# Kernel optimization log

Hardware: AMD Instinct MI355X
Metric: run time of the kernel (lower is better)

Reference implementation:

```python
import jax, jax.numpy as jnp
import numpy as np

HIDDEN = 1024
HEADS = 16
HEAD_DIM = HIDDEN // HEADS


def setup_inputs() -> dict:
    key = jax.random.key(0)
    kx, kw = jax.random.split(key)
    x = jax.random.normal(kx, (1, 4096, HIDDEN), dtype=jnp.float32)
    # torch Linear weight is [out, in]; we store as [in, out] for x @ W
    W_qkv = jax.random.normal(kw, (HIDDEN, 3 * HIDDEN), dtype=jnp.float32) * (HIDDEN ** -0.5)
    return {"x": x, "W_qkv": W_qkv}


def reference(x, W_qkv):
    B, T, _ = x.shape
    qkv = x @ W_qkv                                    # [B, T, 3*HIDDEN]
    qkv = qkv.reshape(B, T, 3, HEADS, HEAD_DIM)
    qkv = jnp.transpose(qkv, (2, 0, 3, 1, 4))          # [3, B, H, T, Dh]
    q, k, v = qkv[0], qkv[1], qkv[2]
    scale = HEAD_DIM ** -0.5
    attn = jnp.einsum("bhqd,bhkd->bhqk", q, k) * scale  # [B, H, T, T] materialized (naive)
    attn = jax.nn.softmax(attn, axis=-1)
    out = jnp.einsum("bhqk,bhkd->bhqd", attn, v)        # [B, H, T, Dh]
    out = jnp.transpose(out, (0, 2, 1, 3)).reshape(B, T, HIDDEN)
    return out
```

## Files before the change

kernel.cpp:

```cpp
#include <hip/hip_runtime.h>

#define SEQ 4096
#define HID 1024
#define NH  16
#define DH  64
#define N3  3072

typedef __attribute__((ext_vector_type(4))) float floatx4;
typedef __attribute__((ext_vector_type(8))) short shortx8;
typedef __attribute__((ext_vector_type(4))) short shortx4;

__device__ __forceinline__ short f2bf(float f) {
    return (short)((__builtin_bit_cast(unsigned, f) + 0x8000u) >> 16);
}
__device__ __forceinline__ unsigned pk2bf(float a, float b) {
    unsigned ua = __builtin_bit_cast(unsigned, a) + 0x8000u;
    unsigned ub = __builtin_bit_cast(unsigned, b) + 0x8000u;
    return (ua >> 16) | (ub & 0xFFFF0000u);
}
__device__ __forceinline__ shortx4 pk4bf(float a, float b, float c, float d) {
    union { unsigned u[2]; shortx4 s; } x;
    x.u[0] = pk2bf(a, b);
    x.u[1] = pk2bf(c, d);
    return x.s;
}

__device__ __forceinline__ unsigned cvtpk(float lo, float hi) {
    unsigned r;
    asm("v_cvt_pk_bf16_f32 %0, %1, %2" : "=v"(r) : "v"(lo), "v"(hi));
    return r;
}

#if __has_builtin(__builtin_amdgcn_exp2f)
#define fexp2 __builtin_amdgcn_exp2f
#else
#define fexp2 exp2f
#endif

#define mfma32 __builtin_amdgcn_mfma_f32_16x16x32_bf16

__device__ __forceinline__ void gll16(const short* g, short* l) {
    __builtin_amdgcn_global_load_lds(
        (const __attribute__((address_space(1))) unsigned*)g,
        (__attribute__((address_space(3))) unsigned*)l, 16, 0, 0);
}

__global__ __launch_bounds__(256) void convert_x(
    const float* __restrict__ x, short* __restrict__ Xb)
{
    size_t i = (size_t)blockIdx.x * 256 + threadIdx.x;
    float4 v = *(const float4*)&x[i * 4];
    shortx4 b = pk4bf(v.x, v.y, v.z, v.w);
    *(shortx4*)&Xb[i * 4] = b;
}

__global__ __launch_bounds__(256) void transpose_W(
    const float* __restrict__ W, short* __restrict__ Wt)
{
    __shared__ short Ws[128 * 40];
    const int t  = threadIdx.x;
    const int n0 = blockIdx.x * 128;
    const int k0 = blockIdx.y * 32;
    #pragma unroll
    for (int i = 0; i < 4; i++) {
        int idx = t + i * 256;
        int k = idx >> 5, c4 = idx & 31;
        float4 v = *(const float4*)&W[(size_t)(k0 + k) * N3 + n0 + c4 * 4];
        Ws[(c4 * 4 + 0) * 40 + k] = f2bf(v.x);
        Ws[(c4 * 4 + 1) * 40 + k] = f2bf(v.y);
        Ws[(c4 * 4 + 2) * 40 + k] = f2bf(v.z);
        Ws[(c4 * 4 + 3) * 40 + k] = f2bf(v.w);
    }
    __syncthreads();
    #pragma unroll
    for (int i = 0; i < 2; i++) {
        int idx = t + i * 256;
        int n = idx >> 2, seg = idx & 3;
        shortx8 g = *(const shortx8*)&Ws[n * 40 + seg * 8];
        *(shortx8*)&Wt[(size_t)(n0 + n) * HID + k0 + seg * 8] = g;
    }
}

#define LDC 136
__global__ __launch_bounds__(256) void qkv_gemm(
    const short* __restrict__ Xb, const short* __restrict__ Wt,
    short* __restrict__ Qb, short* __restrict__ Kb, short* __restrict__ Vb)
{
    __shared__ short SM[18432];
    short* As = SM;
    short* Bs = SM + 128 * 64;
    const int tid  = threadIdx.x;
    const int m0   = blockIdx.x * 128;
    const int n0   = blockIdx.y * 128;
    const int lane = tid & 63;
    const int wid  = tid >> 6;
    const int wm   = (wid >> 1) * 64;
    const int wn   = (wid & 1) * 64;
    const int l15  = lane & 15;
    const int quad = lane >> 4;

    floatx4 acc[4][4];
    #pragma unroll
    for (int i = 0; i < 4; i++)
        #pragma unroll
        for (int j = 0; j < 4; j++)
            acc[i][j] = (floatx4){0.f, 0.f, 0.f, 0.f};

    const int arow = tid >> 3, ac = tid & 7;
    const int swk  = (ac ^ (arow & 7)) << 3;
    const short* ag = Xb + (size_t)(m0 + arow) * HID + swk;
    const short* bg = Wt + (size_t)(n0 + arow) * HID + swk;
    short* al = As + (size_t)(tid & 192) * 8;
    short* bl = Bs + (size_t)(tid & 192) * 8;
    const int r7 = l15 & 7;

    for (int k0 = 0; k0 < HID; k0 += 64) {
        #pragma unroll
        for (int i = 0; i < 4; i++)
            gll16(ag + (size_t)i * 32 * HID + k0, al + i * 2048);
        #pragma unroll
        for (int i = 0; i < 4; i++)
            gll16(bg + (size_t)i * 32 * HID + k0, bl + i * 2048);
        __syncthreads();
        #pragma unroll
        for (int kh = 0; kh < 2; kh++) {
            shortx8 af[4], bf[4];
            #pragma unroll
            for (int t = 0; t < 4; t++) {
                int R = wm + t * 16 + l15;
                af[t] = *(const shortx8*)&As[(R << 6) + ((((kh << 2) + quad) ^ r7) << 3)];
                int Rb = wn + t * 16 + l15;
                bf[t] = *(const shortx8*)&Bs[(Rb << 6) + ((((kh << 2) + quad) ^ r7) << 3)];
            }
            #pragma unroll
            for (int tm = 0; tm < 4; tm++)
                #pragma unroll
                for (int tn = 0; tn < 4; tn++)
                    acc[tm][tn] = mfma32(af[tm], bf[tn], acc[tm][tn], 0, 0, 0);
        }
        __syncthreads();
    }

    short* Cs = SM;
    const float sc = (n0 < 1024) ? 0.18033688011112042f : 1.0f;
    #pragma unroll
    for (int tm = 0; tm < 4; tm++)
        #pragma unroll
        for (int tn = 0; tn < 4; tn++)
            #pragma unroll
            for (int r = 0; r < 4; r++)
                Cs[(wm + tm * 16 + quad * 4 + r) * LDC + wn + tn * 16 + l15] =
                    f2bf(acc[tm][tn][r] * sc);
    __syncthreads();
    short* base = (n0 < 1024) ? Qb : (n0 < 2048 ? Kb : Vb);
    const int h0 = (n0 & 1023) >> 6;
    #pragma unroll
    for (int j = 0; j < 8; j++) {
        int idx = tid + j * 256;
        int row = idx >> 4, col = (idx & 15) * 8;
        shortx8 v = *(const shortx8*)&Cs[row * LDC + col];
        *(shortx8*)&base[((size_t)(h0 + (col >> 6)) * SEQ + m0 + row) * DH + (col & 63)] = v;
    }
}

__global__ __launch_bounds__(256) void transpose_V(
    const short* __restrict__ Vb, short* __restrict__ Vt)
{
    __shared__ short Ts[64 * 72];
    const int t  = threadIdx.x;
    const int t0 = blockIdx.x * 64;
    const int h  = blockIdx.y;
    #pragma unroll
    for (int i = 0; i < 2; i++) {
        int idx = t + i * 256;
        int r = idx >> 3, seg = idx & 7;
        shortx8 g = *(const shortx8*)&Vb[((size_t)h * SEQ + t0 + r) * DH + seg * 8];
        *(shortx8*)&Ts[r * 72 + seg * 8] = g;
    }
    __syncthreads();
    #pragma unroll
    for (int i = 0; i < 2; i++) {
        int idx = t + i * 256;
        int d = idx >> 3, tseg = idx & 7;
        shortx8 g;
        #pragma unroll
        for (int j = 0; j < 8; j++) g[j] = Ts[(tseg * 8 + j) * 72 + d];
        *(shortx8*)&Vt[((size_t)h * DH + d) * SEQ + t0 + tseg * 8] = g;
    }
}

__global__ __launch_bounds__(256) void flash_attn(
    const short* __restrict__ Qb, const short* __restrict__ Kb,
    const short* __restrict__ Vt, float* __restrict__ out,
    float* __restrict__ Opart, float* __restrict__ Lpart,
    int kpc, int nit, int final)
{
    __shared__ short Ks[2][4096];
    __shared__ short Vs[2][4096];
    const int tid  = threadIdx.x;
    const int lane = tid & 63;
    const int l15  = lane & 15;
    const int quad = lane >> 4;

    const int nblk = (int)(gridDim.x * gridDim.y * gridDim.z);
    const int lin  = (int)blockIdx.x + ((int)blockIdx.y << 5) + ((int)blockIdx.z << 9);
    const int work = (lin & 7) * (nblk >> 3) + (lin >> 3);
    const int h    = (work >> 5) & 15;
    const int ch   = work >> 9;
    const int q0   = (work & 31) * 128 + (tid >> 6) * 32;
    const int tstart = ch * kpc;
    const shortx8 ones8 = {(short)0x3F80, (short)0x3F80, (short)0x3F80, (short)0x3F80,
                           (short)0x3F80, (short)0x3F80, (short)0x3F80, (short)0x3F80};

    const short* qp = Qb + ((size_t)h * SEQ + q0 + l15) * DH;
    shortx8 qf00 = *(const shortx8*)(qp + quad * 8);
    shortx8 qf01 = *(const shortx8*)(qp + 32 + quad * 8);
    shortx8 qf10 = *(const shortx8*)(qp + 16 * DH + quad * 8);
    shortx8 qf11 = *(const shortx8*)(qp + 16 * DH + 32 + quad * 8);

    floatx4 oacc[2][4];
    #pragma unroll
    for (int s = 0; s < 2; s++)
        #pragma unroll
        for (int dn = 0; dn < 4; dn++)
            oacc[s][dn] = (floatx4){0.f, 0.f, 0.f, 0.f};
    floatx4 lacc0 = {0.f, 0.f, 0.f, 0.f}, lacc1 = {0.f, 0.f, 0.f, 0.f};

    const int rK   = tid >> 3, sK = tid & 7;
    const int key0 = 8 * ((rK >> 2) & 3) + 4 * ((rK >> 4) & 1) + (rK & 3);
    const int swo  = (sK ^ (rK & 7)) << 3;
    const short* kg = Kb + ((size_t)h * SEQ + tstart + key0) * DH + swo;
    const short* vg = Vt + ((size_t)h * DH + rK) * SEQ + tstart + swo;
    const int wslot = (tid & 192) * 8;

    gll16(kg,            &Ks[0][wslot]);
    gll16(kg + 32 * DH,  &Ks[0][wslot + 2048]);
    gll16(vg,            &Vs[0][wslot]);
    gll16(vg + 32 * SEQ, &Vs[0][wslot + 2048]);
    kg += 64 * DH;  vg += 64;

    for (int it = 0; it < nit; it++) {
        __syncthreads();
        if (it + 1 < nit) {
            int b = (it + 1) & 1;
            gll16(kg,            &Ks[b][wslot]);
            gll16(kg + 32 * DH,  &Ks[b][wslot + 2048]);
            gll16(vg,            &Vs[b][wslot]);
            gll16(vg + 32 * SEQ, &Vs[b][wslot + 2048]);
            kg += 64 * DH;  vg += 64;
        }
        const short* ks = Ks[it & 1];
        const short* vs = Vs[it & 1];

        floatx4 st0[4], st1[4];
        __builtin_amdgcn_s_setprio(1);
        #pragma unroll
        for (int tn = 0; tn < 4; tn++) {
            int R = tn * 16 + l15;
            int off = (R << 6) + ((quad ^ (R & 7)) << 3);
            shortx8 kf0 = *(const shortx8*)&ks[off];
            shortx8 kf1 = *(const shortx8*)&ks[off ^ 32];
            floatx4 a0 = {0.f, 0.f, 0.f, 0.f};
            a0 = mfma32(kf0, qf00, a0, 0, 0, 0);
            a0 = mfma32(kf1, qf01, a0, 0, 0, 0);
            st0[tn] = a0;
            floatx4 a1 = {0.f, 0.f, 0.f, 0.f};
            a1 = mfma32(kf0, qf10, a1, 0, 0, 0);
            a1 = mfma32(kf1, qf11, a1, 0, 0, 0);
            st1[tn] = a1;
        }
        __builtin_amdgcn_s_setprio(0);

        union { unsigned u[4]; shortx8 s; } pa00, pa01, pa10, pa11;
        #pragma unroll
        for (int half = 0; half < 2; half++) {
            int ta = half * 2, tb = half * 2 + 1;
            unsigned* d0 = half ? pa01.u : pa00.u;
            unsigned* d1 = half ? pa11.u : pa10.u;
            d0[0] = cvtpk(fexp2(st0[ta][0]), fexp2(st0[ta][1]));
            d0[1] = cvtpk(fexp2(st0[ta][2]), fexp2(st0[ta][3]));
            d0[2] = cvtpk(fexp2(st0[tb][0]), fexp2(st0[tb][1]));
            d0[3] = cvtpk(fexp2(st0[tb][2]), fexp2(st0[tb][3]));
            d1[0] = cvtpk(fexp2(st1[ta][0]), fexp2(st1[ta][1]));
            d1[1] = cvtpk(fexp2(st1[ta][2]), fexp2(st1[ta][3]));
            d1[2] = cvtpk(fexp2(st1[tb][0]), fexp2(st1[tb][1]));
            d1[3] = cvtpk(fexp2(st1[tb][2]), fexp2(st1[tb][3]));
        }

        __builtin_amdgcn_s_setprio(1);
        lacc0 = mfma32(pa00.s, ones8, lacc0, 0, 0, 0);
        lacc0 = mfma32(pa01.s, ones8, lacc0, 0, 0, 0);
        lacc1 = mfma32(pa10.s, ones8, lacc1, 0, 0, 0);
        lacc1 = mfma32(pa11.s, ones8, lacc1, 0, 0, 0);

        #pragma unroll
        for (int dn = 0; dn < 4; dn++) {
            int row = dn * 16 + l15;
            int off = (row << 6) + ((quad ^ (row & 7)) << 3);
            shortx8 va = *(const shortx8*)&vs[off];
            shortx8 vb = *(const shortx8*)&vs[off ^ 32];
            oacc[0][dn] = mfma32(pa00.s, va, oacc[0][dn], 0, 0, 0);
            oacc[0][dn] = mfma32(pa01.s, vb, oacc[0][dn], 0, 0, 0);
            oacc[1][dn] = mfma32(pa10.s, va, oacc[1][dn], 0, 0, 0);
            oacc[1][dn] = mfma32(pa11.s, vb, oacc[1][dn], 0, 0, 0);
        }
        __builtin_amdgcn_s_setprio(0);
    }

    if (final) {
        #pragma unroll
        for (int r = 0; r < 4; r++) {
            float rl0 = 1.0f / lacc0[r], rl1 = 1.0f / lacc1[r];
            int query = q0 + quad * 4 + r;
            float* d0 = out + (size_t)query * HID + h * DH + l15;
            float* d1 = d0 + (size_t)16 * HID;
            #pragma unroll
            for (int dn = 0; dn < 4; dn++) {
                d0[dn * 16] = oacc[0][dn][r] * rl0;
                d1[dn * 16] = oacc[1][dn][r] * rl1;
            }
        }
    } else {
        #pragma unroll
        for (int r = 0; r < 4; r++) {
            int query = q0 + quad * 4 + r;
            float* d0 = Opart + ((size_t)ch * SEQ + query) * HID + h * DH + l15;
            float* d1 = d0 + (size_t)16 * HID;
            #pragma unroll
            for (int dn = 0; dn < 4; dn++) {
                d0[dn * 16] = oacc[0][dn][r];
                d1[dn * 16] = oacc[1][dn][r];
            }
        }
        if (l15 == 0) {
            float* lp = Lpart + ((size_t)ch * NH + h) * SEQ + q0;
            #pragma unroll
            for (int r = 0; r < 4; r++) {
                lp[quad * 4 + r]      = lacc0[r];
                lp[16 + quad * 4 + r] = lacc1[r];
            }
        }
    }
}

__global__ __launch_bounds__(256) void combine(
    const float* __restrict__ Opart, const float* __restrict__ Lpart,
    float* __restrict__ out, int chn)
{
    size_t i = ((size_t)blockIdx.x * 256 + threadIdx.x) * 4;
    int q = (int)(i >> 10);
    int h = ((int)i & 1023) >> 6;
    float4 o = {0.f, 0.f, 0.f, 0.f};
    float l = 0.f;
    for (int c = 0; c < chn; c++) {
        float4 p = *(const float4*)&Opart[(size_t)c * SEQ * HID + i];
        o.x += p.x; o.y += p.y; o.z += p.z; o.w += p.w;
        l += Lpart[((size_t)c * NH + h) * SEQ + q];
    }
    float rl = 1.0f / l;
    float4 r = {o.x * rl, o.y * rl, o.z * rl, o.w * rl};
    *(float4*)&out[i] = r;
}

extern "C" void kernel_launch(void* const* d_in, const int* in_sizes, int n_in,
                              void* d_out, int out_size, void* d_ws, size_t ws_size,
                              hipStream_t stream) {
    const float* x = (const float*)d_in[0];
    const float* W = (const float*)d_in[1];
    float* out = (float*)d_out;

    short* Xb = (short*)d_ws;
    short* Wt = Xb + (size_t)SEQ * HID;
    short* Qb = Wt + (size_t)N3 * HID;
    short* Kb = Qb + (size_t)NH * SEQ * DH;
    short* Vb = Kb + (size_t)NH * SEQ * DH;
    short* Vt = Xb;
    float* Opart = (float*)(Vb + (size_t)NH * SEQ * DH);

    const size_t need = 39845888ull
                      + 2ull * SEQ * HID * 4
                      + 2ull * NH * SEQ * 4;
    const int chn = (ws_size >= need) ? 2 : 1;
    float* Lpart = Opart + (size_t)chn * SEQ * HID;
    const int kpc = SEQ / chn, nit = kpc / 64;

    convert_x  <<<dim3(SEQ * HID / 1024), 256, 0, stream>>>(x, Xb);
    transpose_W<<<dim3(N3 / 128, HID / 32), 256, 0, stream>>>(W, Wt);
    qkv_gemm   <<<dim3(SEQ / 128, N3 / 128), 256, 0, stream>>>(Xb, Wt, Qb, Kb, Vb);
    transpose_V<<<dim3(SEQ / 64, NH), 256, 0, stream>>>(Vb, Vt);
    flash_attn <<<dim3(SEQ / 128, NH, chn), 256, 0, stream>>>(
        Qb, Kb, Vt, out, Opart, Lpart, kpc, nit, chn == 1);
    if (chn > 1)
        combine<<<dim3(SEQ * HID / 1024), 256, 0, stream>>>(Opart, Lpart, out, chn);
}
```

Baseline: 201.6 us.

## Use two waves of 64 queries per block to double K/V fragment reuse

The flash attention block drops from four waves of 32 queries to two waves of 64 queries each. Every K and V fragment read from shared memory now feeds twice as many MFMAs, which halves LDS read traffic per unit of compute. Each thread now issues eight global-to-LDS loads per stage instead of four. The cost is more accumulator and Q registers per wave and fewer waves per block, which can reduce occupancy and the ability to hide latency.

```diff
diff --git a/kernel.cpp b/kernel.cpp
--- a/kernel.cpp
+++ b/kernel.cpp
@@ -189,7 +189,7 @@
     }
 }
 
-__global__ __launch_bounds__(256) void flash_attn(
+__global__ __launch_bounds__(128, 2) void flash_attn(
     const short* __restrict__ Qb, const short* __restrict__ Kb,
     const short* __restrict__ Vt, float* __restrict__ out,
     float* __restrict__ Opart, float* __restrict__ Lpart,
@@ -198,6 +198,7 @@
     __shared__ short Ks[2][4096];
     __shared__ short Vs[2][4096];
     const int tid  = threadIdx.x;
+    const int wid  = tid >> 6;
     const int lane = tid & 63;
     const int l15  = lane & 15;
     const int quad = lane >> 4;
@@ -207,91 +208,97 @@
     const int work = (lin & 7) * (nblk >> 3) + (lin >> 3);
     const int h    = (work >> 5) & 15;
     const int ch   = work >> 9;
-    const int q0   = (work & 31) * 128 + (tid >> 6) * 32;
+    const int q0   = (work & 31) * 128 + wid * 64;
     const int tstart = ch * kpc;
     const shortx8 ones8 = {(short)0x3F80, (short)0x3F80, (short)0x3F80, (short)0x3F80,
                            (short)0x3F80, (short)0x3F80, (short)0x3F80, (short)0x3F80};
-
-    const short* qp = Qb + ((size_t)h * SEQ + q0 + l15) * DH;
-    shortx8 qf00 = *(const shortx8*)(qp + quad * 8);
-    shortx8 qf01 = *(const shortx8*)(qp + 32 + quad * 8);
-    shortx8 qf10 = *(const shortx8*)(qp + 16 * DH + quad * 8);
-    shortx8 qf11 = *(const shortx8*)(qp + 16 * DH + 32 + quad * 8);
-
-    floatx4 oacc[2][4];
-    #pragma unroll
-    for (int s = 0; s < 2; s++)
+    const floatx4 z4 = {0.f, 0.f, 0.f, 0.f};
+
+    shortx8 qf[4][2];
+    #pragma unroll
+    for (int s = 0; s < 4; s++) {
+        const short* qp = Qb + ((size_t)h * SEQ + q0 + s * 16 + l15) * DH;
+        qf[s][0] = *(const shortx8*)(qp + quad * 8);
+        qf[s][1] = *(const shortx8*)(qp + 32 + quad * 8);
+    }
+
+    floatx4 oacc[4][4];
+    #pragma unroll
+    for (int s = 0; s < 4; s++)
         #pragma unroll
         for (int dn = 0; dn < 4; dn++)
-            oacc[s][dn] = (floatx4){0.f, 0.f, 0.f, 0.f};
-    floatx4 lacc0 = {0.f, 0.f, 0.f, 0.f}, lacc1 = {0.f, 0.f, 0.f, 0.f};
+            oacc[s][dn] = z4;
+    floatx4 lacc[4] = {z4, z4, z4, z4};
 
     const int rK   = tid >> 3, sK = tid & 7;
-    const int key0 = 8 * ((rK >> 2) & 3) + 4 * ((rK >> 4) & 1) + (rK & 3);
+    const int key0 = 8 * ((rK >> 2) & 3) + (rK & 3);
     const int swo  = (sK ^ (rK & 7)) << 3;
     const short* kg = Kb + ((size_t)h * SEQ + tstart + key0) * DH + swo;
     const short* vg = Vt + ((size_t)h * DH + rK) * SEQ + tstart + swo;
-    const int wslot = (tid & 192) * 8;
-
-    gll16(kg,            &Ks[0][wslot]);
-    gll16(kg + 32 * DH,  &Ks[0][wslot + 2048]);
-    gll16(vg,            &Vs[0][wslot]);
-    gll16(vg + 32 * SEQ, &Vs[0][wslot + 2048]);
+    const int wbase = (tid & 64) * 8;
+
+#define STAGE(b) do { \
+        gll16(kg,            &Ks[b][wbase]); \
+        gll16(kg + 4 * DH,   &Ks[b][wbase + 1024]); \
+        gll16(kg + 32 * DH,  &Ks[b][wbase + 2048]); \
+        gll16(kg + 36 * DH,  &Ks[b][wbase + 3072]); \
+        gll16(vg,            &Vs[b][wbase]); \
+        gll16(vg + 16 * SEQ, &Vs[b][wbase + 1024]); \
+        gll16(vg + 32 * SEQ, &Vs[b][wbase + 2048]); \
+        gll16(vg + 48 * SEQ, &Vs[b][wbase + 3072]); \
+    } while (0)
+
+    STAGE(0);
     kg += 64 * DH;  vg += 64;
 
     for (int it = 0; it < nit; it++) {
         __syncthreads();
         if (it + 1 < nit) {
             int b = (it + 1) & 1;
-            gll16(kg,            &Ks[b][wslot]);
-            gll16(kg + 32 * DH,  &Ks[b][wslot + 2048]);
-            gll16(vg,            &Vs[b][wslot]);
-            gll16(vg + 32 * SEQ, &Vs[b][wslot + 2048]);
+            STAGE(b);
             kg += 64 * DH;  vg += 64;
         }
         const short* ks = Ks[it & 1];
         const short* vs = Vs[it & 1];
 
-        floatx4 st0[4], st1[4];
+        union { unsigned u[4]; shortx8 s8; } pa[4][2];
+        #pragma unroll
+        for (int pair = 0; pair < 2; pair++) {
+            int Ra = (pair * 2) * 16 + l15;
+            int Rb = (pair * 2 + 1) * 16 + l15;
+            int offa = (Ra << 6) + ((quad ^ (Ra & 7)) << 3);
+            int offb = (Rb << 6) + ((quad ^ (Rb & 7)) << 3);
+            shortx8 kf0a = *(const shortx8*)&ks[offa];
+            shortx8 kf1a = *(const shortx8*)&ks[offa ^ 32];
+            shortx8 kf0b = *(const shortx8*)&ks[offb];
+            shortx8 kf1b = *(const shortx8*)&ks[offb ^ 32];
+            floatx4 sta[4], stb[4];
+            __builtin_amdgcn_s_setprio(1);
+            #pragma unroll
+            for (int s = 0; s < 4; s++) {
+                floatx4 a = mfma32(kf0a, qf[s][0], z4, 0, 0, 0);
+                a = mfma32(kf1a, qf[s][1], a, 0, 0, 0);
+                sta[s] = a;
+                floatx4 b = mfma32(kf0b, qf[s][0], z4, 0, 0, 0);
+                b = mfma32(kf1b, qf[s][1], b, 0, 0, 0);
+                stb[s] = b;
+            }
+            __builtin_amdgcn_s_setprio(0);
+            #pragma unroll
+            for (int s = 0; s < 4; s++) {
+                pa[s][pair].u[0] = cvtpk(fexp2(sta[s][0]), fexp2(sta[s][1]));
+                pa[s][pair].u[1] = cvtpk(fexp2(sta[s][2]), fexp2(sta[s][3]));
+                pa[s][pair].u[2] = cvtpk(fexp2(stb[s][0]), fexp2(stb[s][1]));
+                pa[s][pair].u[3] = cvtpk(fexp2(stb[s][2]), fexp2(stb[s][3]));
+            }
+        }
+
         __builtin_amdgcn_s_setprio(1);
         #pragma unroll
-        for (int tn = 0; tn < 4; tn++) {
-            int R = tn * 16 + l15;
-            int off = (R << 6) + ((quad ^ (R & 7)) << 3);
-            shortx8 kf0 = *(const shortx8*)&ks[off];
-            shortx8 kf1 = *(const shortx8*)&ks[off ^ 32];
-            floatx4 a0 = {0.f, 0.f, 0.f, 0.f};
-            a0 = mfma32(kf0, qf00, a0, 0, 0, 0);
-            a0 = mfma32(kf1, qf01, a0, 0, 0, 0);
-            st0[tn] = a0;
-            floatx4 a1 = {0.f, 0.f, 0.f, 0.f};
-            a1 = mfma32(kf0, qf10, a1, 0, 0, 0);
-            a1 = mfma32(kf1, qf11, a1, 0, 0, 0);
-            st1[tn] = a1;
-        }
-        __builtin_amdgcn_s_setprio(0);
-
-        union { unsigned u[4]; shortx8 s; } pa00, pa01, pa10, pa11;
-        #pragma unroll
-        for (int half = 0; half < 2; half++) {
-            int ta = half * 2, tb = half * 2 + 1;
-            unsigned* d0 = half ? pa01.u : pa00.u;
-            unsigned* d1 = half ? pa11.u : pa10.u;
-            d0[0] = cvtpk(fexp2(st0[ta][0]), fexp2(st0[ta][1]));
-            d0[1] = cvtpk(fexp2(st0[ta][2]), fexp2(st0[ta][3]));
-            d0[2] = cvtpk(fexp2(st0[tb][0]), fexp2(st0[tb][1]));
-            d0[3] = cvtpk(fexp2(st0[tb][2]), fexp2(st0[tb][3]));
-            d1[0] = cvtpk(fexp2(st1[ta][0]), fexp2(st1[ta][1]));
-            d1[1] = cvtpk(fexp2(st1[ta][2]), fexp2(st1[ta][3]));
-            d1[2] = cvtpk(fexp2(st1[tb][0]), fexp2(st1[tb][1]));
-            d1[3] = cvtpk(fexp2(st1[tb][2]), fexp2(st1[tb][3]));
-        }
-
-        __builtin_amdgcn_s_setprio(1);
-        lacc0 = mfma32(pa00.s, ones8, lacc0, 0, 0, 0);
-        lacc0 = mfma32(pa01.s, ones8, lacc0, 0, 0, 0);
-        lacc1 = mfma32(pa10.s, ones8, lacc1, 0, 0, 0);
-        lacc1 = mfma32(pa11.s, ones8, lacc1, 0, 0, 0);
+        for (int s = 0; s < 4; s++) {
+            lacc[s] = mfma32(pa[s][0].s8, ones8, lacc[s], 0, 0, 0);
+            lacc[s] = mfma32(pa[s][1].s8, ones8, lacc[s], 0, 0, 0);
+        }
 
         #pragma unroll
         for (int dn = 0; dn < 4; dn++) {
@@ -299,46 +306,46 @@
             int off = (row << 6) + ((quad ^ (row & 7)) << 3);
             shortx8 va = *(const shortx8*)&vs[off];
             shortx8 vb = *(const shortx8*)&vs[off ^ 32];
-            oacc[0][dn] = mfma32(pa00.s, va, oacc[0][dn], 0, 0, 0);
-            oacc[0][dn] = mfma32(pa01.s, vb, oacc[0][dn], 0, 0, 0);
-            oacc[1][dn] = mfma32(pa10.s, va, oacc[1][dn], 0, 0, 0);
-            oacc[1][dn] = mfma32(pa11.s, vb, oacc[1][dn], 0, 0, 0);
+            #pragma unroll
+            for (int s = 0; s < 4; s++) {
+                oacc[s][dn] = mfma32(pa[s][0].s8, va, oacc[s][dn], 0, 0, 0);
+                oacc[s][dn] = mfma32(pa[s][1].s8, vb, oacc[s][dn], 0, 0, 0);
+            }
         }
         __builtin_amdgcn_s_setprio(0);
     }
+#undef STAGE
 
     if (final) {
         #pragma unroll
-        for (int r = 0; r < 4; r++) {
-            float rl0 = 1.0f / lacc0[r], rl1 = 1.0f / lacc1[r];
-            int query = q0 + quad * 4 + r;
-            float* d0 = out + (size_t)query * HID + h * DH + l15;
-            float* d1 = d0 + (size_t)16 * HID;
-            #pragma unroll
-            for (int dn = 0; dn < 4; dn++) {
-                d0[dn * 16] = oacc[0][dn][r] * rl0;
-                d1[dn * 16] = oacc[1][dn][r] * rl1;
-            }
-        }
+        for (int s = 0; s < 4; s++)
+            #pragma unroll
+            for (int r = 0; r < 4; r++) {
+                float rl = 1.0f / lacc[s][r];
+                int query = q0 + s * 16 + quad * 4 + r;
+                float* d = out + (size_t)query * HID + h * DH + l15;
+                #pragma unroll
+                for (int dn = 0; dn < 4; dn++)
+                    d[dn * 16] = oacc[s][dn][r] * rl;
+            }
     } else {
         #pragma unroll
-        for (int r = 0; r < 4; r++) {
-            int query = q0 + quad * 4 + r;
-            float* d0 = Opart + ((size_t)ch * SEQ + query) * HID + h * DH + l15;
-            float* d1 = d0 + (size_t)16 * HID;
-            #pragma unroll
-            for (int dn = 0; dn < 4; dn++) {
-                d0[dn * 16] = oacc[0][dn][r];
-                d1[dn * 16] = oacc[1][dn][r];
-            }
-        }
+        for (int s = 0; s < 4; s++)
+            #pragma unroll
+            for (int r = 0; r < 4; r++) {
+                int query = q0 + s * 16 + quad * 4 + r;
+                float* d = Opart + ((size_t)ch * SEQ + query) * HID + h * DH + l15;
+                #pragma unroll
+                for (int dn = 0; dn < 4; dn++)
+                    d[dn * 16] = oacc[s][dn][r];
+            }
         if (l15 == 0) {
             float* lp = Lpart + ((size_t)ch * NH + h) * SEQ + q0;
             #pragma unroll
-            for (int r = 0; r < 4; r++) {
-                lp[quad * 4 + r]      = lacc0[r];
-                lp[16 + quad * 4 + r] = lacc1[r];
-            }
+            for (int s = 0; s < 4; s++)
+                #pragma unroll
+                for (int r = 0; r < 4; r++)
+                    lp[s * 16 + quad * 4 + r] = lacc[s][r];
         }
     }
 }
@@ -388,7 +395,7 @@
     transpose_W<<<dim3(N3 / 128, HID / 32), 256, 0, stream>>>(W, Wt);
     qkv_gemm   <<<dim3(SEQ / 128, N3 / 128), 256, 0, stream>>>(Xb, Wt, Qb, Kb, Vb);
     transpose_V<<<dim3(SEQ / 64, NH), 256, 0, stream>>>(Vb, Vt);
-    flash_attn <<<dim3(SEQ / 128, NH, chn), 256, 0, stream>>>(
+    flash_attn <<<dim3(SEQ / 128, NH, chn), 128, 0, stream>>>(
         Qb, Kb, Vt, out, Opart, Lpart, kpc, nit, chn == 1);
     if (chn > 1)
         combine<<<dim3(SEQ * HID / 1024), 256, 0, stream>>>(Opart, Lpart, out, chn);
```

After: 202.6 us. No clear change (+0.5%).
